# Kernel tuning notes

Measured on AMD Instinct MI355X. Metric: run time of the kernel, lower is better.

The kernel has to match this reference:

```python
import jax, jax.numpy as jnp
import numpy as np

S, B, D_IN, D_SRC, D_ALIGN = 2048, 64, 512, 512, 512


def setup_inputs() -> dict:
    key = jax.random.key(0)
    ks = jax.random.split(key, 6)
    scale = 0.1  # matches uniform_(-0.1, 0.1) init magnitude
    return {
        "input": jax.random.normal(ks[0], (1, B, D_IN), dtype=jnp.float32),
        "source_hids": jax.random.normal(ks[1], (S, B, D_SRC), dtype=jnp.float32),
        "encoder_padding_mask": jnp.zeros((S, B), dtype=bool),
        "W1": jax.random.uniform(ks[2], (D_ALIGN, D_IN + D_SRC), jnp.float32, -scale, scale),
        "b1": jax.random.uniform(ks[3], (D_ALIGN,), jnp.float32, -scale, scale),
        "W2": jax.random.uniform(ks[4], (1, D_ALIGN), jnp.float32, -scale, scale),
        "b2": jax.random.uniform(ks[5], (1,), jnp.float32, -scale, scale),
    }


def reference(input, source_hids, encoder_padding_mask, W1, b1, W2, b2):
    # input: [1, B, D_in] broadcast over srclen; source_hids: [S, B, D_src]
    s = source_hids.shape[0]
    x = jnp.broadcast_to(input, (s,) + input.shape[1:])          # [S, B, D_in]
    cat = jnp.concatenate((x, source_hids), axis=-1)             # [S, B, D_in+D_src]
    h = jnp.tanh(jnp.einsum('sbd,ad->sba', cat, W1) + b1)        # [S, B, D_align]
    scores = jnp.einsum('sba,oa->sbo', h, W2)[..., 0] + b2[0]    # [S, B]
    scores = jnp.where(encoder_padding_mask, -jnp.inf, scores)
    attn = jax.nn.softmax(scores, axis=0)                        # softmax over srclen
    ctx = jnp.einsum('sb,sbd->bd', attn, source_hids)            # [B, D_src]
    return ctx, attn
```

## Files before the change

### kernel.cpp

```cpp
#include <hip/hip_runtime.h>
#include <hip/hip_bf16.h>
#include <math.h>

#define S_LEN 2048
#define BATCH 64
#define DDIM 512

typedef __attribute__((ext_vector_type(8))) short bf16x8;
typedef __attribute__((ext_vector_type(4))) float f32x4;
typedef __attribute__((ext_vector_type(4))) unsigned int u32x4;

__device__ __forceinline__ unsigned short f2bf(float f) {
  unsigned int u = __float_as_uint(f);
  u += 0x7fffu + ((u >> 16) & 1u);
  return (unsigned short)(u >> 16);
}

__device__ __forceinline__ float tanh_fast(float x) {
  float e = __builtin_amdgcn_exp2f(x * 2.88539008177793f);
  return 1.0f - 2.0f * __builtin_amdgcn_rcpf(e + 1.0f);
}

__device__ __forceinline__ unsigned pkbf(float a, float b) {
  unsigned ua = __float_as_uint(a) + 0x8000u;
  unsigned ub = __float_as_uint(b) + 0x8000u;
  return __builtin_amdgcn_perm(ub, ua, 0x07060302u);
}

__global__ __launch_bounds__(256) void prep_kernel(
    const float* __restrict__ W1, const float* __restrict__ b1,
    const float* __restrict__ input, unsigned short* __restrict__ W1bT,
    float* __restrict__ uprime) {
  __shared__ float w1row[1024];
  const int a = blockIdx.x;
  const int t = threadIdx.x;
  float4 v = *(const float4*)(W1 + a * 1024 + t * 4);
  *(float4*)(w1row + t * 4) = v;
  if (t >= 128) {
    ushort4 u;
    u.x = f2bf(v.x); u.y = f2bf(v.y); u.z = f2bf(v.z); u.w = f2bf(v.w);
    const int d = t * 4 - 512;
    const int kc = d >> 3;
    const int e = d & 7;
    *(ushort4*)(W1bT + ((size_t)kc * 512 + a) * 8 + e) = u;
  }
  __syncthreads();
  if (t < BATCH) {
    const float4* inp = (const float4*)(input + t * 512);
    const float4* wr = (const float4*)w1row;
    float acc = b1[a];
#pragma unroll 4
    for (int d = 0; d < 128; ++d) {
      float4 x = inp[d], w = wr[d];
      acc += x.x * w.x + x.y * w.y + x.z * w.z + x.w * w.w;
    }
    uprime[t * 512 + a] = acc;
  }
}

__global__ __launch_bounds__(256, 2) void scores_kernel(
    const float* __restrict__ src, const unsigned short* __restrict__ W1bT,
    const float* __restrict__ uprime, const float* __restrict__ W2,
    float* __restrict__ scores_t) {
  __shared__ unsigned short A_sm[64 * 512];
  __shared__ float s_lds[BATCH];

  const int t = threadIdx.x;
  const int s = blockIdx.x;
  const int w = t >> 6;
  const int lane = t & 63;
  const int quad = lane >> 4;
  const int l15 = lane & 15;

  if (t < BATCH) s_lds[t] = 0.f;

  f32x4 acc[4][8];
#pragma unroll
  for (int i = 0; i < 4; ++i)
#pragma unroll
    for (int j = 0; j < 8; ++j) acc[i][j] = (f32x4){0.f, 0.f, 0.f, 0.f};

  {
    const float4* gsrc = (const float4*)(src + (size_t)s * (BATCH * DDIM));
    const int cc = t & 63;
#pragma unroll 4
    for (int n = 0; n < 16; ++n) {
      const int row = n * 4 + (t >> 6);
      const float4 v0 = gsrc[row * 128 + cc * 2];
      const float4 v1 = gsrc[row * 128 + cc * 2 + 1];
      u32x4 o;
      o.x = pkbf(v0.x, v0.y);
      o.y = pkbf(v0.z, v0.w);
      o.z = pkbf(v1.x, v1.y);
      o.w = pkbf(v1.z, v1.w);
      const int p = cc ^ (row & 7);
      *(u32x4*)(A_sm + row * 512 + p * 8) = o;
    }
  }
  __syncthreads();

  const unsigned short* gB = W1bT + ((size_t)quad * 512 + w * 128 + l15) * 8;
#pragma unroll 4
  for (int n = 0; n < 16; ++n) {
    bf16x8 bb[8], af[4];
#pragma unroll
    for (int j = 0; j < 8; ++j)
      bb[j] = *(const bf16x8*)(gB + ((size_t)n * 4 * 512 + j * 16) * 8);
    const int c = n * 4 + quad;
#pragma unroll
    for (int i = 0; i < 4; ++i) {
      const int r = i * 16 + l15;
      af[i] = *(const bf16x8*)(A_sm + r * 512 + ((c ^ (r & 7)) << 3));
    }
#pragma unroll
    for (int i = 0; i < 4; ++i)
#pragma unroll
      for (int j = 0; j < 8; ++j)
        acc[i][j] = __builtin_amdgcn_mfma_f32_16x16x32_bf16(af[i], bb[j],
                                                            acc[i][j], 0, 0, 0);
  }

  float w2r[8];
#pragma unroll
  for (int j = 0; j < 8; ++j) w2r[j] = W2[w * 128 + j * 16 + l15];

#pragma unroll
  for (int i = 0; i < 4; ++i) {
#pragma unroll
    for (int r = 0; r < 4; ++r) {
      const int b = i * 16 + quad * 4 + r;
      const float* up = uprime + b * 512 + w * 128 + l15;
      float sp = 0.f;
#pragma unroll
      for (int j = 0; j < 8; ++j)
        sp += w2r[j] * tanh_fast(acc[i][j][r] + up[j * 16]);
      sp += __shfl_xor(sp, 1);
      sp += __shfl_xor(sp, 2);
      sp += __shfl_xor(sp, 4);
      sp += __shfl_xor(sp, 8);
      if (l15 == 0) atomicAdd(&s_lds[b], sp);
    }
  }
  __syncthreads();
  if (t < BATCH) scores_t[t * S_LEN + s] = s_lds[t];
}

__global__ __launch_bounds__(256) void softmax_kernel(
    const float* __restrict__ scores_t, const unsigned char* __restrict__ mask,
    float* __restrict__ attn_g, float* __restrict__ attn_t, int write_t) {
  __shared__ float red[256];
  const int b = blockIdx.x, t = threadIdx.x;
  float m = -__builtin_inff();
  float sc[8];
#pragma unroll
  for (int c = 0; c < 8; ++c) {
    const int s = t + c * 256;
    sc[c] = mask[s * BATCH + b] ? -__builtin_inff() : scores_t[b * S_LEN + s];
    m = fmaxf(m, sc[c]);
  }
  red[t] = m;
  __syncthreads();
  for (int off = 128; off; off >>= 1) {
    if (t < off) red[t] = fmaxf(red[t], red[t + off]);
    __syncthreads();
  }
  m = red[0];
  __syncthreads();
  float sum = 0.f;
#pragma unroll
  for (int c = 0; c < 8; ++c) sum += __expf(sc[c] - m);
  red[t] = sum;
  __syncthreads();
  for (int off = 128; off; off >>= 1) {
    if (t < off) red[t] += red[t + off];
    __syncthreads();
  }
  const float inv = 1.f / red[0];
#pragma unroll
  for (int c = 0; c < 8; ++c) {
    const int s = t + c * 256;
    const float p = __expf(sc[c] - m) * inv;
    attn_g[s * BATCH + b] = p;
    if (write_t) attn_t[b * S_LEN + s] = p;
  }
}

__global__ __launch_bounds__(256) void ctx_partial_kernel(
    const float* __restrict__ src, const float* __restrict__ attn_t,
    float* __restrict__ partial) {
  __shared__ float a_lds[64];
  const int c = blockIdx.x;
  const int b = blockIdx.y;
  const int t = threadIdx.x;
  if (t < 64) a_lds[t] = attn_t[b * S_LEN + c * 64 + t];
  __syncthreads();
  const int f4i = t & 127;
  const int sh = t >> 7;
  const float4* base =
      (const float4*)src + ((size_t)(c * 64 + sh * 32) * BATCH + b) * 128 + f4i;
  float4 acc = {0.f, 0.f, 0.f, 0.f};
#pragma unroll 8
  for (int i = 0; i < 32; ++i) {
    const float a = a_lds[sh * 32 + i];
    float4 v = base[(size_t)i * BATCH * 128];
    acc.x += a * v.x; acc.y += a * v.y; acc.z += a * v.z; acc.w += a * v.w;
  }
  ((float4*)partial)[((size_t)(c * 2 + sh) * BATCH + b) * 128 + f4i] = acc;
}

__global__ __launch_bounds__(256) void ctx_reduce_kernel(
    const float* __restrict__ partial, float* __restrict__ ctx) {
  const int b = blockIdx.x, t = threadIdx.x;
  const float2* p = (const float2*)partial + (size_t)b * 256 + t;
  float2 acc = {0.f, 0.f};
#pragma unroll 8
  for (int c2 = 0; c2 < 64; ++c2) {
    float2 v = p[(size_t)c2 * BATCH * 256];
    acc.x += v.x; acc.y += v.y;
  }
  ((float2*)ctx)[b * 256 + t] = acc;
}

__global__ __launch_bounds__(256) void ctx_atomic_kernel(
    const float* __restrict__ src, const float* __restrict__ attn_g,
    float* __restrict__ ctx) {
  __shared__ float a_lds[128];
  const int s0 = blockIdx.x * 128, b = blockIdx.y, t = threadIdx.x;
  if (t < 128) a_lds[t] = attn_g[(s0 + t) * BATCH + b];
  __syncthreads();
  const int f4i = t & 127;
  const int sh = t >> 7;
  const float4* base =
      (const float4*)src + ((size_t)(s0 + sh * 64) * BATCH + b) * 128 + f4i;
  float4 acc = {0.f, 0.f, 0.f, 0.f};
#pragma unroll 8
  for (int i = 0; i < 64; ++i) {
    const float a = a_lds[sh * 64 + i];
    float4 v = base[(size_t)i * BATCH * 128];
    acc.x += a * v.x; acc.y += a * v.y; acc.z += a * v.z; acc.w += a * v.w;
  }
  float* cp = ctx + b * DDIM + f4i * 4;
  atomicAdd(cp + 0, acc.x);
  atomicAdd(cp + 1, acc.y);
  atomicAdd(cp + 2, acc.z);
  atomicAdd(cp + 3, acc.w);
}

extern "C" void kernel_launch(void* const* d_in, const int* in_sizes, int n_in,
                              void* d_out, int out_size, void* d_ws, size_t ws_size,
                              hipStream_t stream) {
  const float* input = (const float*)d_in[0];
  const float* src = (const float*)d_in[1];
  const unsigned char* mask = (const unsigned char*)d_in[2];
  const float* W1 = (const float*)d_in[3];
  const float* b1 = (const float*)d_in[4];
  const float* W2 = (const float*)d_in[5];

  float* ctx = (float*)d_out;
  float* attn = (float*)d_out + BATCH * DDIM;

  unsigned short* W1bT = (unsigned short*)d_ws;
  float* uprime = (float*)((char*)d_ws + 512 * 1024);
  float* scores_t = (float*)((char*)d_ws + 640 * 1024);
  float* attn_t = (float*)((char*)d_ws + 1152 * 1024);
  float* partial = (float*)((char*)d_ws + 1664 * 1024);
  const size_t NEED_ATTN_T = 1664 * 1024;
  const size_t NEED_PARTIAL = 1664 * 1024 + (size_t)64 * BATCH * DDIM * 4;
  const int have_attn_t = ws_size >= NEED_ATTN_T;
  const int have_partial = ws_size >= NEED_PARTIAL;

  prep_kernel<<<512, 256, 0, stream>>>(W1, b1, input, W1bT, uprime);
  scores_kernel<<<S_LEN, 256, 0, stream>>>(src, W1bT, uprime, W2, scores_t);
  softmax_kernel<<<BATCH, 256, 0, stream>>>(scores_t, mask, attn, attn_t,
                                            have_attn_t && have_partial);
  if (have_partial) {
    ctx_partial_kernel<<<dim3(32, BATCH), 256, 0, stream>>>(src, attn_t, partial);
    ctx_reduce_kernel<<<BATCH, 256, 0, stream>>>(partial, ctx);
  } else {
    hipMemsetAsync(ctx, 0, BATCH * DDIM * sizeof(float), stream);
    ctx_atomic_kernel<<<dim3(16, BATCH), 256, 0, stream>>>(src, attn, ctx);
  }
}
```

Measured before the change: 506.0 us.

## Split scores GEMM into two column passes with double-buffered fragment loads

Each wave now covers its 128 align columns in two passes of 64, which halves the live accumulator registers. Within a pass, B and A fragments are double-buffered in software so loads overlap MFMAs. MFMA issue runs at raised priority, and adjacent blocks stagger their K order to spread L2 traffic on W1. The trade-off is that the tanh/W2 epilogue runs twice and the A fragments are read from LDS twice, which adds some LDS traffic.

```diff
diff --git a/kernel.cpp b/kernel.cpp
--- a/kernel.cpp
+++ b/kernel.cpp
@@ -71,14 +71,9 @@
   const int lane = t & 63;
   const int quad = lane >> 4;
   const int l15 = lane & 15;
+  const int stag8 = (s & 1) << 3;
 
   if (t < BATCH) s_lds[t] = 0.f;
-
-  f32x4 acc[4][8];
-#pragma unroll
-  for (int i = 0; i < 4; ++i)
-#pragma unroll
-    for (int j = 0; j < 8; ++j) acc[i][j] = (f32x4){0.f, 0.f, 0.f, 0.f};
 
   {
     const float4* gsrc = (const float4*)(src + (size_t)s * (BATCH * DDIM));
@@ -99,48 +94,81 @@
   }
   __syncthreads();
 
-  const unsigned short* gB = W1bT + ((size_t)quad * 512 + w * 128 + l15) * 8;
-#pragma unroll 4
-  for (int n = 0; n < 16; ++n) {
-    bf16x8 bb[8], af[4];
-#pragma unroll
-    for (int j = 0; j < 8; ++j)
-      bb[j] = *(const bf16x8*)(gB + ((size_t)n * 4 * 512 + j * 16) * 8);
-    const int c = n * 4 + quad;
+#define LOADB(dst, nn, pcol)                                                   \
+  {                                                                            \
+    const int kcb = ((nn) ^ stag8) * 4 + quad;                                 \
+    _Pragma("unroll") for (int j_ = 0; j_ < 4; ++j_) dst[j_] =                 \
+        *(const bf16x8*)(W1bT + ((size_t)kcb * 512 + (pcol) + j_ * 16) * 8);   \
+  }
+#define LOADA(dst, nn)                                                         \
+  {                                                                            \
+    const int cb = ((nn) ^ stag8) * 4 + quad;                                  \
+    _Pragma("unroll") for (int i_ = 0; i_ < 4; ++i_) {                         \
+      const int r_ = i_ * 16 + l15;                                            \
+      dst[i_] = *(const bf16x8*)(A_sm + r_ * 512 + ((cb ^ (r_ & 7)) << 3));    \
+    }                                                                          \
+  }
+#define MFMA16(af, bb)                                                         \
+  {                                                                            \
+    __builtin_amdgcn_s_setprio(1);                                             \
+    _Pragma("unroll") for (int i_ = 0; i_ < 4; ++i_)                           \
+        _Pragma("unroll") for (int j_ = 0; j_ < 4; ++j_) acc[i_][j_] =         \
+            __builtin_amdgcn_mfma_f32_16x16x32_bf16(af[i_], bb[j_],            \
+                                                    acc[i_][j_], 0, 0, 0);     \
+    __builtin_amdgcn_s_setprio(0);                                             \
+  }
+
+#pragma unroll
+  for (int p = 0; p < 2; ++p) {
+    const int pcol = p * 256 + w * 64 + l15;
+
+    f32x4 acc[4][4];
+#pragma unroll
+    for (int i = 0; i < 4; ++i)
+#pragma unroll
+      for (int j = 0; j < 4; ++j) acc[i][j] = (f32x4){0.f, 0.f, 0.f, 0.f};
+
+    bf16x8 bbA[4], bbB[4], afA[4], afB[4];
+    LOADB(bbA, 0, pcol);
+    LOADA(afA, 0);
+#pragma unroll
+    for (int n = 0; n < 16; n += 2) {
+      LOADB(bbB, n + 1, pcol);
+      LOADA(afB, n + 1);
+      MFMA16(afA, bbA);
+      if (n + 2 < 16) {
+        LOADB(bbA, n + 2, pcol);
+        LOADA(afA, n + 2);
+      }
+      MFMA16(afB, bbB);
+    }
+
+    float w2r[4];
+#pragma unroll
+    for (int j = 0; j < 4; ++j) w2r[j] = W2[pcol + j * 16];
+
 #pragma unroll
     for (int i = 0; i < 4; ++i) {
-      const int r = i * 16 + l15;
-      af[i] = *(const bf16x8*)(A_sm + r * 512 + ((c ^ (r & 7)) << 3));
+#pragma unroll
+      for (int r = 0; r < 4; ++r) {
+        const int b = i * 16 + quad * 4 + r;
+        const float* up = uprime + b * 512 + pcol;
+        float sp = 0.f;
+#pragma unroll
+        for (int j = 0; j < 4; ++j)
+          sp += w2r[j] * tanh_fast(acc[i][j][r] + up[j * 16]);
+        sp += __shfl_xor(sp, 1);
+        sp += __shfl_xor(sp, 2);
+        sp += __shfl_xor(sp, 4);
+        sp += __shfl_xor(sp, 8);
+        if (l15 == 0) atomicAdd(&s_lds[b], sp);
+      }
     }
-#pragma unroll
-    for (int i = 0; i < 4; ++i)
-#pragma unroll
-      for (int j = 0; j < 8; ++j)
-        acc[i][j] = __builtin_amdgcn_mfma_f32_16x16x32_bf16(af[i], bb[j],
-                                                            acc[i][j], 0, 0, 0);
-  }
-
-  float w2r[8];
-#pragma unroll
-  for (int j = 0; j < 8; ++j) w2r[j] = W2[w * 128 + j * 16 + l15];
-
-#pragma unroll
-  for (int i = 0; i < 4; ++i) {
-#pragma unroll
-    for (int r = 0; r < 4; ++r) {
-      const int b = i * 16 + quad * 4 + r;
-      const float* up = uprime + b * 512 + w * 128 + l15;
-      float sp = 0.f;
-#pragma unroll
-      for (int j = 0; j < 8; ++j)
-        sp += w2r[j] * tanh_fast(acc[i][j][r] + up[j * 16]);
-      sp += __shfl_xor(sp, 1);
-      sp += __shfl_xor(sp, 2);
-      sp += __shfl_xor(sp, 4);
-      sp += __shfl_xor(sp, 8);
-      if (l15 == 0) atomicAdd(&s_lds[b], sp);
-    }
-  }
+  }
+#undef LOADB
+#undef LOADA
+#undef MFMA16
+
   __syncthreads();
   if (t < BATCH) scores_t[t * S_LEN + s] = s_lds[t];
 }
```

After: 526.0 us. +4.0%, slower.

## Fuse scores, chunk-local softmax and context accumulation into one flash-style kernel

Applied to the files above, without the earlier changes.

Each block of the scores kernel now handles one batch and a 64-position chunk instead of one source position across the whole batch. It computes the scores, a chunk-local max and exp-sum, and the weighted partial context while that source slice is still fresh in cache. A small combine kernel then rescales the partials to give the final ctx and the attention output. This removes the separate softmax, ctx_partial and ctx_reduce passes and the second full read of source_hids. The cost is per-row strided loads of src in the GEMM staging and the online-softmax bookkeeping.

```diff
diff --git a/kernel.cpp b/kernel.cpp
--- a/kernel.cpp
+++ b/kernel.cpp
@@ -58,21 +58,25 @@
   }
 }
 
-__global__ __launch_bounds__(256, 2) void scores_kernel(
+__global__ __launch_bounds__(256, 2) void fused_kernel(
     const float* __restrict__ src, const unsigned short* __restrict__ W1bT,
     const float* __restrict__ uprime, const float* __restrict__ W2,
-    float* __restrict__ scores_t) {
+    const unsigned char* __restrict__ mask, float* __restrict__ scores_t,
+    float* __restrict__ ml, float* __restrict__ partialO, int wpart) {
   __shared__ unsigned short A_sm[64 * 512];
-  __shared__ float s_lds[BATCH];
+  __shared__ float s_sc[64];
+  __shared__ float s_p[64];
+  __shared__ float4 s_O[2][128];
 
   const int t = threadIdx.x;
-  const int s = blockIdx.x;
+  const int b = blockIdx.x & 63;
+  const int c = blockIdx.x >> 6;
   const int w = t >> 6;
   const int lane = t & 63;
   const int quad = lane >> 4;
   const int l15 = lane & 15;
 
-  if (t < BATCH) s_lds[t] = 0.f;
+  if (t < 64) s_sc[t] = 0.f;
 
   f32x4 acc[4][8];
 #pragma unroll
@@ -81,13 +85,14 @@
     for (int j = 0; j < 8; ++j) acc[i][j] = (f32x4){0.f, 0.f, 0.f, 0.f};
 
   {
-    const float4* gsrc = (const float4*)(src + (size_t)s * (BATCH * DDIM));
+    const float4* sf4 = (const float4*)src;
     const int cc = t & 63;
 #pragma unroll 4
     for (int n = 0; n < 16; ++n) {
       const int row = n * 4 + (t >> 6);
-      const float4 v0 = gsrc[row * 128 + cc * 2];
-      const float4 v1 = gsrc[row * 128 + cc * 2 + 1];
+      const float4* grow = sf4 + ((size_t)(c * 64 + row) * 64 + b) * 128;
+      const float4 v0 = grow[cc * 2];
+      const float4 v1 = grow[cc * 2 + 1];
       u32x4 o;
       o.x = pkbf(v0.x, v0.y);
       o.y = pkbf(v0.z, v0.w);
@@ -106,11 +111,11 @@
 #pragma unroll
     for (int j = 0; j < 8; ++j)
       bb[j] = *(const bf16x8*)(gB + ((size_t)n * 4 * 512 + j * 16) * 8);
-    const int c = n * 4 + quad;
+    const int cch = n * 4 + quad;
 #pragma unroll
     for (int i = 0; i < 4; ++i) {
       const int r = i * 16 + l15;
-      af[i] = *(const bf16x8*)(A_sm + r * 512 + ((c ^ (r & 7)) << 3));
+      af[i] = *(const bf16x8*)(A_sm + r * 512 + ((cch ^ (r & 7)) << 3));
     }
 #pragma unroll
     for (int i = 0; i < 4; ++i)
@@ -120,34 +125,121 @@
                                                             acc[i][j], 0, 0, 0);
   }
 
-  float w2r[8];
-#pragma unroll
-  for (int j = 0; j < 8; ++j) w2r[j] = W2[w * 128 + j * 16 + l15];
+  float w2r[8], upr[8];
+#pragma unroll
+  for (int j = 0; j < 8; ++j) {
+    w2r[j] = W2[w * 128 + j * 16 + l15];
+    upr[j] = uprime[b * 512 + w * 128 + j * 16 + l15];
+  }
 
 #pragma unroll
   for (int i = 0; i < 4; ++i) {
 #pragma unroll
     for (int r = 0; r < 4; ++r) {
-      const int b = i * 16 + quad * 4 + r;
-      const float* up = uprime + b * 512 + w * 128 + l15;
+      const int sl = i * 16 + quad * 4 + r;
       float sp = 0.f;
 #pragma unroll
       for (int j = 0; j < 8; ++j)
-        sp += w2r[j] * tanh_fast(acc[i][j][r] + up[j * 16]);
+        sp += w2r[j] * tanh_fast(acc[i][j][r] + upr[j]);
       sp += __shfl_xor(sp, 1);
       sp += __shfl_xor(sp, 2);
       sp += __shfl_xor(sp, 4);
       sp += __shfl_xor(sp, 8);
-      if (l15 == 0) atomicAdd(&s_lds[b], sp);
-    }
-  }
-  __syncthreads();
-  if (t < BATCH) scores_t[t * S_LEN + s] = s_lds[t];
+      if (l15 == 0) atomicAdd(&s_sc[sl], sp);
+    }
+  }
+  __syncthreads();
+
+  if (t < 64) {
+    float sc = s_sc[t];
+    if (mask[(size_t)(c * 64 + t) * BATCH + b]) sc = -__builtin_inff();
+    s_sc[t] = sc;
+    scores_t[b * S_LEN + c * 64 + t] = sc;
+  }
+  __syncthreads();
+  float mc = -__builtin_inff();
+#pragma unroll
+  for (int k = 0; k < 64; ++k) mc = fmaxf(mc, s_sc[k]);
+  if (t < 64) {
+    const float sc = s_sc[t];
+    s_p[t] = (mc == -__builtin_inff()) ? 0.f : __expf(sc - mc);
+  }
+  __syncthreads();
+  if (wpart && t == 0) {
+    float l = 0.f;
+#pragma unroll
+    for (int k = 0; k < 64; ++k) l += s_p[k];
+    ml[(b * 32 + c) * 2] = mc;
+    ml[(b * 32 + c) * 2 + 1] = l;
+  }
+
+  if (!wpart) return;
+
+  {
+    const int f4i = t & 127;
+    const int sh = t >> 7;
+    const float4* base =
+        (const float4*)src + ((size_t)(c * 64 + sh * 32) * 64 + b) * 128 + f4i;
+    float4 a4 = {0.f, 0.f, 0.f, 0.f};
+#pragma unroll 8
+    for (int i = 0; i < 32; ++i) {
+      const float p = s_p[sh * 32 + i];
+      float4 v = base[(size_t)i * 8192];
+      a4.x += p * v.x; a4.y += p * v.y; a4.z += p * v.z; a4.w += p * v.w;
+    }
+    s_O[sh][f4i] = a4;
+  }
+  __syncthreads();
+  if (t < 128) {
+    float4 o0 = s_O[0][t], o1 = s_O[1][t];
+    float4 o = {o0.x + o1.x, o0.y + o1.y, o0.z + o1.z, o0.w + o1.w};
+    ((float4*)partialO)[(size_t)(b * 32 + c) * 128 + t] = o;
+  }
+}
+
+__global__ __launch_bounds__(256) void combine_kernel(
+    const float* __restrict__ scores_t, const float* __restrict__ ml,
+    const float* __restrict__ partialO, float* __restrict__ ctx,
+    float* __restrict__ attn) {
+  __shared__ float sm[32], sl[32], ss[32];
+  const int b = blockIdx.x, t = threadIdx.x;
+  if (t < 32) {
+    sm[t] = ml[(b * 32 + t) * 2];
+    sl[t] = ml[(b * 32 + t) * 2 + 1];
+  }
+  __syncthreads();
+  float m = -__builtin_inff();
+#pragma unroll
+  for (int c = 0; c < 32; ++c) m = fmaxf(m, sm[c]);
+  if (t < 32) ss[t] = (sl[t] > 0.f) ? __expf(sm[t] - m) : 0.f;
+  __syncthreads();
+  float L = 0.f;
+#pragma unroll
+  for (int c = 0; c < 32; ++c) L += sl[c] * ss[c];
+  const float invL = 1.f / L;
+
+  float2 a = {0.f, 0.f};
+  const float2* po = (const float2*)partialO + (size_t)b * 32 * 256 + t;
+#pragma unroll 8
+  for (int c = 0; c < 32; ++c) {
+    float2 v = po[c * 256];
+    a.x += ss[c] * v.x;
+    a.y += ss[c] * v.y;
+  }
+  float2 o = {a.x * invL, a.y * invL};
+  ((float2*)ctx)[b * 256 + t] = o;
+
+#pragma unroll
+  for (int k = 0; k < 8; ++k) {
+    const int s = k * 256 + t;
+    const float p = __expf(scores_t[b * S_LEN + s] - m) * invL;
+    attn[s * BATCH + b] = p;
+  }
 }
 
 __global__ __launch_bounds__(256) void softmax_kernel(
     const float* __restrict__ scores_t, const unsigned char* __restrict__ mask,
-    float* __restrict__ attn_g, float* __restrict__ attn_t, int write_t) {
+    float* __restrict__ attn_g) {
   __shared__ float red[256];
   const int b = blockIdx.x, t = threadIdx.x;
   float m = -__builtin_inff();
@@ -179,46 +271,8 @@
 #pragma unroll
   for (int c = 0; c < 8; ++c) {
     const int s = t + c * 256;
-    const float p = __expf(sc[c] - m) * inv;
-    attn_g[s * BATCH + b] = p;
-    if (write_t) attn_t[b * S_LEN + s] = p;
-  }
-}
-
-__global__ __launch_bounds__(256) void ctx_partial_kernel(
-    const float* __restrict__ src, const float* __restrict__ attn_t,
-    float* __restrict__ partial) {
-  __shared__ float a_lds[64];
-  const int c = blockIdx.x;
-  const int b = blockIdx.y;
-  const int t = threadIdx.x;
-  if (t < 64) a_lds[t] = attn_t[b * S_LEN + c * 64 + t];
-  __syncthreads();
-  const int f4i = t & 127;
-  const int sh = t >> 7;
-  const float4* base =
-      (const float4*)src + ((size_t)(c * 64 + sh * 32) * BATCH + b) * 128 + f4i;
-  float4 acc = {0.f, 0.f, 0.f, 0.f};
-#pragma unroll 8
-  for (int i = 0; i < 32; ++i) {
-    const float a = a_lds[sh * 32 + i];
-    float4 v = base[(size_t)i * BATCH * 128];
-    acc.x += a * v.x; acc.y += a * v.y; acc.z += a * v.z; acc.w += a * v.w;
-  }
-  ((float4*)partial)[((size_t)(c * 2 + sh) * BATCH + b) * 128 + f4i] = acc;
-}
-
-__global__ __launch_bounds__(256) void ctx_reduce_kernel(
-    const float* __restrict__ partial, float* __restrict__ ctx) {
-  const int b = blockIdx.x, t = threadIdx.x;
-  const float2* p = (const float2*)partial + (size_t)b * 256 + t;
-  float2 acc = {0.f, 0.f};
-#pragma unroll 8
-  for (int c2 = 0; c2 < 64; ++c2) {
-    float2 v = p[(size_t)c2 * BATCH * 256];
-    acc.x += v.x; acc.y += v.y;
-  }
-  ((float2*)ctx)[b * 256 + t] = acc;
+    attn_g[s * BATCH + b] = __expf(sc[c] - m) * inv;
+  }
 }
 
 __global__ __launch_bounds__(256) void ctx_atomic_kernel(
@@ -262,21 +316,18 @@
   unsigned short* W1bT = (unsigned short*)d_ws;
   float* uprime = (float*)((char*)d_ws + 512 * 1024);
   float* scores_t = (float*)((char*)d_ws + 640 * 1024);
-  float* attn_t = (float*)((char*)d_ws + 1152 * 1024);
-  float* partial = (float*)((char*)d_ws + 1664 * 1024);
-  const size_t NEED_ATTN_T = 1664 * 1024;
-  const size_t NEED_PARTIAL = 1664 * 1024 + (size_t)64 * BATCH * DDIM * 4;
-  const int have_attn_t = ws_size >= NEED_ATTN_T;
-  const int have_partial = ws_size >= NEED_PARTIAL;
+  float* ml = (float*)((char*)d_ws + 1152 * 1024);
+  float* partialO = (float*)((char*)d_ws + 1168 * 1024);
+  const size_t NEED_FUSED = 1168 * 1024 + (size_t)64 * 32 * 512 * 4;
+  const int wpart = ws_size >= NEED_FUSED;
 
   prep_kernel<<<512, 256, 0, stream>>>(W1, b1, input, W1bT, uprime);
-  scores_kernel<<<S_LEN, 256, 0, stream>>>(src, W1bT, uprime, W2, scores_t);
-  softmax_kernel<<<BATCH, 256, 0, stream>>>(scores_t, mask, attn, attn_t,
-                                            have_attn_t && have_partial);
-  if (have_partial) {
-    ctx_partial_kernel<<<dim3(32, BATCH), 256, 0, stream>>>(src, attn_t, partial);
-    ctx_reduce_kernel<<<BATCH, 256, 0, stream>>>(partial, ctx);
+  fused_kernel<<<2048, 256, 0, stream>>>(src, W1bT, uprime, W2, mask, scores_t,
+                                         ml, partialO, wpart);
+  if (wpart) {
+    combine_kernel<<<BATCH, 256, 0, stream>>>(scores_t, ml, partialO, ctx, attn);
   } else {
+    softmax_kernel<<<BATCH, 256, 0, stream>>>(scores_t, mask, attn);
     hipMemsetAsync(ctx, 0, BATCH * DDIM * sizeof(float), stream);
     ctx_atomic_kernel<<<dim3(16, BATCH), 256, 0, stream>>>(src, attn, ctx);
   }
```

Measured after the change: 477.0 us. 5.7% less time.
